# Kernel optimization log

Hardware: AMD Instinct MI355X
Metric: run time of the kernel (lower is better)

## Reference

```python
import jax, jax.numpy as jnp
import numpy as np

N, E = 50000, 800000
C, A_ALL, RAD_IN, FC1, FC2 = 128, 256, 32, 64, 64
H, AH, VH = 8, 16, 16  # heads, alpha channels/head, value channels/head


def _radial_mlp(x, w1, b1, w2, b2, w3, b3):
    x = jax.nn.silu(x @ w1 + b1)
    x = jax.nn.silu(x @ w2 + b2)
    return x @ w3 + b3


def _smooth_leaky_relu(x, a=0.2):
    # Equiformer SmoothLeakyReLU: 0.5*(1+a)*x + 0.5*(1-a)*x*(2*sigmoid(x)-1)
    return 0.5 * (1.0 + a) * x + 0.5 * (1.0 - a) * x * (2.0 * jax.nn.sigmoid(x) - 1.0)


def _segment_softmax(scores, seg, num_segments):
    m = jax.ops.segment_max(scores, seg, num_segments=num_segments)
    m = jnp.where(jnp.isfinite(m), m, 0.0)
    e = jnp.exp(scores - m[seg])
    s = jax.ops.segment_sum(e, seg, num_segments=num_segments)
    return e / (s[seg] + 1e-16)


def setup_inputs():
    key = jax.random.key(0)
    ks = jax.random.split(key, 16)

    def g(k, shape):
        scale = 1.0 / np.sqrt(shape[0])
        return jax.random.normal(k, shape, dtype=jnp.float32) * scale

    return {
        "node_input": jax.random.normal(ks[0], (N, C), dtype=jnp.float32),
        "node_attr": jnp.ones((N, 1), jnp.float32),
        "edge_attr": jax.random.uniform(ks[1], (E, 1), dtype=jnp.float32),
        "edge_scalars": jax.random.normal(ks[2], (E, RAD_IN), dtype=jnp.float32),
        "edge_src": jax.random.randint(ks[3], (E,), 0, N, dtype=jnp.int32),
        "edge_dst": jax.random.randint(ks[4], (E,), 0, N, dtype=jnp.int32),
        "batch": jnp.zeros((N,), jnp.int32),
        "w_src": g(ks[5], (C, C)), "b_src": jnp.zeros((C,), jnp.float32),
        "w_dst": g(ks[6], (C, C)),
        "fc_w1": g(ks[7], (RAD_IN, FC1)), "fc_b1": jnp.zeros((FC1,), jnp.float32),
        "fc_w2": g(ks[8], (FC1, FC2)), "fc_b2": jnp.zeros((FC2,), jnp.float32),
        "fc_w3": g(ks[9], (FC2, C)), "fc_b3": jnp.zeros((C,), jnp.float32),
        "w_sep": g(ks[10], (C, A_ALL)), "b_sep": jnp.zeros((A_ALL,), jnp.float32),
        "alpha_dot": jax.random.normal(ks[11], (1, H, AH), dtype=jnp.float32) * np.sqrt(2.0 / (H * AH)),
        "w_proj": g(ks[12], (H * VH, C)), "b_proj": jnp.zeros((C,), jnp.float32),
    }


def reference(node_input, node_attr, edge_attr, edge_scalars, edge_src, edge_dst, batch,
              w_src, b_src, w_dst, fc_w1, fc_b1, fc_w2, fc_b2, fc_w3, fc_b3,
              w_sep, b_sep, alpha_dot, w_proj, b_proj):
    n_nodes = node_input.shape[0]
    n_edges = edge_src.shape[0]
    # merge_src / merge_dst (LinearRS; bias only on src)
    msg_src = node_input @ w_src + b_src                     # [N, C]
    msg_dst = node_input @ w_dst                             # [N, C]
    message = msg_src[edge_src] + msg_dst[edge_dst]          # [E, C] edge gather
    # SeparableFCTP: radial-weighted depthwise tensor product (scalar irreps)
    rad_w = _radial_mlp(edge_scalars, fc_w1, fc_b1, fc_w2, fc_b2, fc_w3, fc_b3)  # [E, C]
    message = message * edge_attr * rad_w                    # depthwise TP
    message = message @ w_sep + b_sep                        # [E, A_ALL] linear to attn_all
    # Vec2AttnHeads + split alpha/value per head
    msg_h = message.reshape(n_edges, H, AH + VH)
    alpha = _smooth_leaky_relu(msg_h[:, :, :AH])             # [E, H, AH]
    value = msg_h[:, :, AH:]                                 # [E, H, VH]
    score = jnp.einsum('ehk,ahk->eh', alpha, alpha_dot)      # [E, H]
    att = _segment_softmax(score, edge_dst, n_nodes)[..., None]
    out = jax.ops.segment_sum(value * att, edge_dst, num_segments=n_nodes)  # scatter-add
    out = out.reshape(n_nodes, H * VH)                       # AttnHeads2Vec
    return out @ w_proj + b_proj
```

## Files before the change

kernel.cpp:

```cpp
#include <hip/hip_runtime.h>

#define NN 50000
#define NE 800000

typedef unsigned short u16;
typedef __bf16 bf16x8 __attribute__((ext_vector_type(8)));
typedef float f32x4 __attribute__((ext_vector_type(4)));

__device__ __forceinline__ u16 f2b(float f){
  unsigned x = __float_as_uint(f);
  return (u16)((x + 0x7FFFu + ((x>>16)&1u)) >> 16);
}
#define MFMA16(a,b,c) __builtin_amdgcn_mfma_f32_16x16x32_bf16((a),(b),(c),0,0,0)

__global__ void k_prep(const float* __restrict__ w1, const float* __restrict__ w2,
                       const float* __restrict__ w3, const float* __restrict__ wsep,
                       const float* __restrict__ wsrc, const float* __restrict__ wdst,
                       const float* __restrict__ wproj,
                       u16* __restrict__ w1T, u16* __restrict__ w2T,
                       u16* __restrict__ w3T, u16* __restrict__ wsepT,
                       u16* __restrict__ wsrcT, u16* __restrict__ wdstT,
                       u16* __restrict__ wprojT)
{
  int id = blockIdx.x*256 + threadIdx.x;
  if (id < 2048)  { int n=id>>5,  k=id&31;  w1T[id]   = f2b(w1[k*64+n]);    return; } id -= 2048;
  if (id < 4096)  { int n=id>>6,  k=id&63;  w2T[id]   = f2b(w2[k*64+n]);    return; } id -= 4096;
  if (id < 8192)  { int n=id>>6,  k=id&63;  w3T[id]   = f2b(w3[k*128+n]);   return; } id -= 8192;
  if (id < 32768) { int n=id>>7,  k=id&127; wsepT[id] = f2b(wsep[k*256+n]); return; } id -= 32768;
  if (id < 16384) { int n=id>>7,  k=id&127; wsrcT[id] = f2b(wsrc[k*128+n]); return; } id -= 16384;
  if (id < 16384) { int n=id>>7,  k=id&127; wdstT[id] = f2b(wdst[k*128+n]); return; } id -= 16384;
  if (id < 16384) { int n=id>>7,  k=id&127; wprojT[id]= f2b(wproj[k*128+n]); return; }
}

__launch_bounds__(256)
__global__ void k_node(const float* __restrict__ x, const u16* __restrict__ wsrcT,
                       const u16* __restrict__ wdstT, const float* __restrict__ bsrc,
                       float* __restrict__ msgsrc, float* __restrict__ msgdst)
{
  __shared__ u16 sX[64*136];
  __shared__ u16 sW[128*136];
  __shared__ float sB[128];
  const int tid = threadIdx.x;
  const int n0 = blockIdx.x*64;
  for (int idx = tid; idx < 64*32; idx += 256){
    int r = idx>>5, s = idx&31;
    float4 v = make_float4(0.f,0.f,0.f,0.f);
    if (n0 + r < NN) v = *(const float4*)(x + (size_t)(n0+r)*128 + s*4);
    ushort4 o; o.x=f2b(v.x); o.y=f2b(v.y); o.z=f2b(v.z); o.w=f2b(v.w);
    *(ushort4*)(&sX[r*136 + s*4]) = o;
  }
  const int wave = tid>>6, lane = tid&63, l15 = lane&15, q = lane>>4;
  for (int half = 0; half < 2; ++half){
    const u16* wT = half ? wdstT : wsrcT;
    for (int idx = tid; idx < 128*16; idx += 256){
      int r = idx>>4, s = idx&15;
      *(uint4*)(&sW[r*136 + s*8]) = *(const uint4*)(wT + r*128 + s*8);
    }
    if (tid < 128) sB[tid] = half ? 0.0f : bsrc[tid];
    __syncthreads();
    f32x4 acc[8];
    #pragma unroll
    for (int n=0;n<8;++n) acc[n] = (f32x4){0.f,0.f,0.f,0.f};
    #pragma unroll
    for (int k0=0;k0<128;k0+=32){
      bf16x8 a = *(const bf16x8*)(&sX[(wave*16+l15)*136 + k0 + q*8]);
      #pragma unroll
      for (int n=0;n<8;++n){
        bf16x8 b = *(const bf16x8*)(&sW[(n*16+l15)*136 + k0 + q*8]);
        acc[n] = MFMA16(a,b,acc[n]);
      }
    }
    float* outp = half ? msgdst : msgsrc;
    #pragma unroll
    for (int n=0;n<8;++n){
      #pragma unroll
      for (int r=0;r<4;++r){
        int row = n0 + wave*16 + q*4 + r;
        if (row < NN) outp[(size_t)row*128 + n*16 + l15] = acc[n][r] + sB[n*16+l15];
      }
    }
    __syncthreads();
  }
}

#define PM 136
#define PH 72
#define PX 40
__launch_bounds__(256)
__global__ void k_edge(const float* __restrict__ escal, const float* __restrict__ eattr,
                       const int* __restrict__ esrc, const int* __restrict__ edst,
                       const float* __restrict__ msgsrc, const float* __restrict__ msgdst,
                       const u16* __restrict__ w1T, const u16* __restrict__ w2T,
                       const u16* __restrict__ w3T, const u16* __restrict__ wsepT,
                       const float* __restrict__ b1, const float* __restrict__ b2,
                       const float* __restrict__ b3, const float* __restrict__ bsep,
                       const float* __restrict__ adot,
                       float* __restrict__ num, float* __restrict__ denom)
{
  __shared__ __attribute__((aligned(16))) char pool[49408];
  u16*   sXs  = (u16*)(pool + 0);
  u16*   sW1  = (u16*)(pool + 5120);
  u16*   sW2  = (u16*)(pool + 10240);
  u16*   sH1  = (u16*)(pool + 19456);
  u16*   sMsg = (u16*)(pool + 28672);
  float* sB1  = (float*)(pool + 46080);
  float* sB2  = (float*)(pool + 46336);
  float* sB3  = (float*)(pool + 46592);
  float* sBs  = (float*)(pool + 47104);
  float* sAD  = (float*)(pool + 48128);
  float* sEA  = (float*)(pool + 48640);
  int*   sSrc = (int*)(pool + 48896);
  int*   sDst = (int*)(pool + 49152);
  u16*   sH2  = (u16*)(pool + 0);
  u16*   sW3C = (u16*)(pool + 10240);
  u16*   sWsp = (u16*)(pool + 10240);

  const int tid = threadIdx.x;
  const int e0 = blockIdx.x*64;
  const int wave = tid>>6, lane = tid&63, l15 = lane&15, q = lane>>4;

  {
    for (int j = tid; j < 512; j += 256){ int r=j>>3, s=j&7;
      float4 v = *(const float4*)(escal + (size_t)(e0+r)*32 + s*4);
      ushort4 o; o.x=f2b(v.x); o.y=f2b(v.y); o.z=f2b(v.z); o.w=f2b(v.w);
      *(ushort4*)&sXs[r*PX + s*4] = o; }
    if (tid < 256){ int r=tid>>2, s=tid&3;
      *(uint4*)&sW1[r*PX + s*8] = *(const uint4*)(w1T + r*32 + s*8); }
    for (int j = tid; j < 512; j += 256){ int r=j>>3, s=j&7;
      *(uint4*)&sW2[r*PH + s*8] = *(const uint4*)(w2T + r*64 + s*8); }
    if (tid < 64)  sB1[tid] = b1[tid];
    if (tid < 64)  sB2[tid] = b2[tid];
    if (tid < 128) sB3[tid] = b3[tid];
    sBs[tid] = bsep[tid];
    if (tid < 128) sAD[tid] = adot[tid];
    if (tid < 64){ sEA[tid] = eattr[e0+tid]; sSrc[tid] = esrc[e0+tid]; sDst[tid] = edst[e0+tid]; }
  }
  __syncthreads();

  {
    f32x4 acc[4];
    #pragma unroll
    for (int n=0;n<4;++n) acc[n] = (f32x4){0.f,0.f,0.f,0.f};
    bf16x8 a = *(const bf16x8*)&sXs[(wave*16+l15)*PX + q*8];
    #pragma unroll
    for (int n=0;n<4;++n){
      bf16x8 b = *(const bf16x8*)&sW1[(n*16+l15)*PX + q*8];
      acc[n] = MFMA16(a,b,acc[n]);
    }
    #pragma unroll
    for (int n=0;n<4;++n){
      #pragma unroll
      for (int r=0;r<4;++r){
        float v = acc[n][r] + sB1[n*16+l15];
        float h = v / (1.0f + __expf(-v));
        sH1[(wave*16+q*4+r)*PH + n*16+l15] = f2b(h);
      }
    }
  }
  __syncthreads();

  {
    f32x4 acc[4];
    #pragma unroll
    for (int n=0;n<4;++n) acc[n] = (f32x4){0.f,0.f,0.f,0.f};
    #pragma unroll
    for (int k0=0;k0<64;k0+=32){
      bf16x8 a = *(const bf16x8*)&sH1[(wave*16+l15)*PH + k0 + q*8];
      #pragma unroll
      for (int n=0;n<4;++n){
        bf16x8 b = *(const bf16x8*)&sW2[(n*16+l15)*PH + k0 + q*8];
        acc[n] = MFMA16(a,b,acc[n]);
      }
    }
    #pragma unroll
    for (int n=0;n<4;++n){
      #pragma unroll
      for (int r=0;r<4;++r){
        float v = acc[n][r] + sB2[n*16+l15];
        float h = v / (1.0f + __expf(-v));
        sH2[(wave*16+q*4+r)*PH + n*16+l15] = f2b(h);
      }
    }
  }
  __syncthreads();

  for (int ch=0; ch<2; ++ch){
    for (int j = tid; j < 512; j += 256){ int r=j>>3, s=j&7;
      *(uint4*)&sW3C[r*PH + s*8] = *(const uint4*)(w3T + (size_t)(ch*64+r)*64 + s*8); }
    __syncthreads();
    const int m0 = (wave&1)*2, n0 = (wave>>1)*2;
    f32x4 acc[2][2];
    #pragma unroll
    for (int mm=0;mm<2;++mm)
      #pragma unroll
      for (int nn=0;nn<2;++nn) acc[mm][nn] = (f32x4){0.f,0.f,0.f,0.f};
    #pragma unroll
    for (int k0=0;k0<64;k0+=32){
      bf16x8 a0 = *(const bf16x8*)&sH2[((m0  )*16+l15)*PH + k0 + q*8];
      bf16x8 a1 = *(const bf16x8*)&sH2[((m0+1)*16+l15)*PH + k0 + q*8];
      bf16x8 b0 = *(const bf16x8*)&sW3C[((n0  )*16+l15)*PH + k0 + q*8];
      bf16x8 b1 = *(const bf16x8*)&sW3C[((n0+1)*16+l15)*PH + k0 + q*8];
      acc[0][0] = MFMA16(a0,b0,acc[0][0]);
      acc[1][0] = MFMA16(a1,b0,acc[1][0]);
      acc[0][1] = MFMA16(a0,b1,acc[0][1]);
      acc[1][1] = MFMA16(a1,b1,acc[1][1]);
    }
    #pragma unroll
    for (int mm=0;mm<2;++mm){
      #pragma unroll
      for (int nn=0;nn<2;++nn){
        int c = ch*64 + (n0+nn)*16 + l15;
        #pragma unroll
        for (int r=0;r<4;++r){
          float v = acc[mm][nn][r] + sB3[c];
          sMsg[((m0+mm)*16+q*4+r)*PM + c] = f2b(v);
        }
      }
    }
    __syncthreads();
  }

  for (int idx = tid; idx < 64*32; idx += 256){
    int r = idx>>5, s = idx&31;
    int cs = s*4;
    float4 a4 = *(const float4*)(msgsrc + (size_t)sSrc[r]*128 + cs);
    float4 d4 = *(const float4*)(msgdst + (size_t)sDst[r]*128 + cs);
    float ea = sEA[r];
    ushort4 rw = *(ushort4*)&sMsg[r*PM + cs];
    ushort4 o;
    o.x = f2b((a4.x + d4.x) * ea * __uint_as_float(((unsigned)rw.x)<<16));
    o.y = f2b((a4.y + d4.y) * ea * __uint_as_float(((unsigned)rw.y)<<16));
    o.z = f2b((a4.z + d4.z) * ea * __uint_as_float(((unsigned)rw.z)<<16));
    o.w = f2b((a4.w + d4.w) * ea * __uint_as_float(((unsigned)rw.w)<<16));
    *(ushort4*)&sMsg[r*PM + cs] = o;
  }
  __syncthreads();

  const int fm0 = (wave&1)*2, fn0 = (wave>>1)*2;
  for (int ch=0; ch<4; ++ch){
    for (int j = tid; j < 1024; j += 256){ int r=j>>4, s=j&15;
      *(uint4*)&sWsp[r*PM + s*8] = *(const uint4*)(wsepT + (size_t)(ch*64+r)*128 + s*8); }
    __syncthreads();
    f32x4 acc[2][2];
    #pragma unroll
    for (int mm=0;mm<2;++mm)
      #pragma unroll
      for (int nn=0;nn<2;++nn) acc[mm][nn] = (f32x4){0.f,0.f,0.f,0.f};
    #pragma unroll
    for (int k0=0;k0<128;k0+=32){
      bf16x8 a0 = *(const bf16x8*)&sMsg[((fm0  )*16+l15)*PM + k0 + q*8];
      bf16x8 a1 = *(const bf16x8*)&sMsg[((fm0+1)*16+l15)*PM + k0 + q*8];
      bf16x8 b0 = *(const bf16x8*)&sWsp[((fn0  )*16+l15)*PM + k0 + q*8];
      bf16x8 b1 = *(const bf16x8*)&sWsp[((fn0+1)*16+l15)*PM + k0 + q*8];
      acc[0][0] = MFMA16(a0,b0,acc[0][0]);
      acc[1][0] = MFMA16(a1,b0,acc[1][0]);
      acc[0][1] = MFMA16(a0,b1,acc[0][1]);
      acc[1][1] = MFMA16(a1,b1,acc[1][1]);
    }
    {
      const int h  = ch*2 + (fn0>>1);
      const int ca = ch*64 + fn0*16;
      const float ba = sBs[ca + l15];
      const float bv = sBs[ca + 16 + l15];
      const float ad = sAD[h*16 + l15];
      #pragma unroll
      for (int mm=0;mm<2;++mm){
        #pragma unroll
        for (int r=0;r<4;++r){
          int eloc = (fm0+mm)*16 + q*4 + r;
          float av  = acc[mm][0][r] + ba;
          float sig = 1.0f/(1.0f + __expf(-av));
          float sl  = av*(0.2f + 0.8f*sig);
          float contrib = sl * ad;
          contrib += __shfl_xor(contrib, 1);
          contrib += __shfl_xor(contrib, 2);
          contrib += __shfl_xor(contrib, 4);
          contrib += __shfl_xor(contrib, 8);
          float w  = __expf(contrib);
          int dst  = sDst[eloc];
          float vv = acc[mm][1][r] + bv;
          unsafeAtomicAdd(&num[(size_t)dst*128 + h*16 + l15], w*vv);
          if (l15 == 0) unsafeAtomicAdd(&denom[(size_t)dst*8 + h], w);
        }
      }
    }
    __syncthreads();
  }
}

__launch_bounds__(256)
__global__ void k_out(const float* __restrict__ num, const float* __restrict__ denom,
                      const u16* __restrict__ wprojT, const float* __restrict__ bproj,
                      float* __restrict__ out)
{
  __shared__ u16 sX[64*136];
  __shared__ u16 sW[128*136];
  __shared__ float sB[128];
  const int tid = threadIdx.x;
  const int n0 = blockIdx.x*64;
  for (int idx = tid; idx < 64*128; idx += 256){
    int r = idx>>7, c = idx&127;
    float xv = 0.f;
    int row = n0 + r;
    if (row < NN){
      float d = denom[row*8 + (c>>4)];
      xv = num[(size_t)row*128 + c] / (d + 1e-16f);
    }
    sX[r*136 + c] = f2b(xv);
  }
  for (int idx = tid; idx < 128*16; idx += 256){ int r=idx>>4, s=idx&15;
    *(uint4*)&sW[r*136 + s*8] = *(const uint4*)(wprojT + r*128 + s*8); }
  if (tid < 128) sB[tid] = bproj[tid];
  __syncthreads();
  const int wave = tid>>6, lane = tid&63, l15 = lane&15, q = lane>>4;
  f32x4 acc[8];
  #pragma unroll
  for (int n=0;n<8;++n) acc[n] = (f32x4){0.f,0.f,0.f,0.f};
  #pragma unroll
  for (int k0=0;k0<128;k0+=32){
    bf16x8 a = *(const bf16x8*)&sX[(wave*16+l15)*136 + k0 + q*8];
    #pragma unroll
    for (int n=0;n<8;++n){
      bf16x8 b = *(const bf16x8*)&sW[(n*16+l15)*136 + k0 + q*8];
      acc[n] = MFMA16(a,b,acc[n]);
    }
  }
  #pragma unroll
  for (int n=0;n<8;++n){
    #pragma unroll
    for (int r=0;r<4;++r){
      int row = n0 + wave*16 + q*4 + r;
      if (row < NN) out[(size_t)row*128 + n*16 + l15] = acc[n][r] + sB[n*16+l15];
    }
  }
}

extern "C" void kernel_launch(void* const* d_in, const int* in_sizes, int n_in,
                              void* d_out, int out_size, void* d_ws, size_t ws_size,
                              hipStream_t stream)
{
  const float* node_input = (const float*)d_in[0];
  const float* eattr = (const float*)d_in[2];
  const float* escal = (const float*)d_in[3];
  const int*   esrc  = (const int*)d_in[4];
  const int*   edst  = (const int*)d_in[5];
  const float* wsrc  = (const float*)d_in[7];
  const float* bsrc  = (const float*)d_in[8];
  const float* wdst  = (const float*)d_in[9];
  const float* w1    = (const float*)d_in[10];
  const float* b1    = (const float*)d_in[11];
  const float* w2    = (const float*)d_in[12];
  const float* b2    = (const float*)d_in[13];
  const float* w3    = (const float*)d_in[14];
  const float* b3    = (const float*)d_in[15];
  const float* wsep  = (const float*)d_in[16];
  const float* bsep  = (const float*)d_in[17];
  const float* adot  = (const float*)d_in[18];
  const float* wproj = (const float*)d_in[19];
  const float* bproj = (const float*)d_in[20];

  char* ws = (char*)d_ws;
  size_t off = 0;
  auto alloc = [&](size_t bytes)->void*{ void* p = ws + off; off += (bytes + 255) & ~(size_t)255; return p; };
  float* msgsrc = (float*)alloc((size_t)NN*128*4);
  float* msgdst = (float*)alloc((size_t)NN*128*4);
  float* num    = (float*)alloc((size_t)NN*128*4);
  float* denom  = (float*)alloc((size_t)NN*8*4);
  u16* w1T    = (u16*)alloc(2048*2);
  u16* w2T    = (u16*)alloc(4096*2);
  u16* w3T    = (u16*)alloc(8192*2);
  u16* wsepT  = (u16*)alloc(32768*2);
  u16* wsrcT  = (u16*)alloc(16384*2);
  u16* wdstT  = (u16*)alloc(16384*2);
  u16* wprojT = (u16*)alloc(16384*2);

  hipMemsetAsync(num,   0, (size_t)NN*128*4, stream);
  hipMemsetAsync(denom, 0, (size_t)NN*8*4,   stream);

  k_prep<<<376, 256, 0, stream>>>(w1,w2,w3,wsep,wsrc,wdst,wproj,
                                  w1T,w2T,w3T,wsepT,wsrcT,wdstT,wprojT);
  k_node<<<782, 256, 0, stream>>>(node_input, wsrcT, wdstT, bsrc, msgsrc, msgdst);
  k_edge<<<12500, 256, 0, stream>>>(escal, eattr, esrc, edst, msgsrc, msgdst,
                                    w1T, w2T, w3T, wsepT, b1, b2, b3, bsep, adot,
                                    num, denom);
  k_out<<<782, 256, 0, stream>>>(num, denom, wprojT, bproj, (float*)d_out);
}
```

Before: 912.8 us.

## Read edge-kernel weights from global memory and shrink LDS for occupancy

Weight matrices, biases and edge index/attr arrays are no longer staged in shared memory. MFMA B operands and biases now come straight from global/L2, which cuts LDS from about 48KB to 26KB and removes several per-chunk __syncthreads. Launch bounds now request 6 blocks per SM to raise occupancy. In exchange, weights are loaded redundantly from global by every wave, and the register cap may cause spills.

```diff
diff --git a/kernel.cpp b/kernel.cpp
--- a/kernel.cpp
+++ b/kernel.cpp
@@ -86,7 +86,7 @@
 #define PM 136
 #define PH 72
 #define PX 40
-__launch_bounds__(256)
+__launch_bounds__(256,6)
 __global__ void k_edge(const float* __restrict__ escal, const float* __restrict__ eattr,
                        const int* __restrict__ esrc, const int* __restrict__ edst,
                        const float* __restrict__ msgsrc, const float* __restrict__ msgdst,
@@ -97,44 +97,20 @@
                        const float* __restrict__ adot,
                        float* __restrict__ num, float* __restrict__ denom)
 {
-  __shared__ __attribute__((aligned(16))) char pool[49408];
-  u16*   sXs  = (u16*)(pool + 0);
-  u16*   sW1  = (u16*)(pool + 5120);
-  u16*   sW2  = (u16*)(pool + 10240);
-  u16*   sH1  = (u16*)(pool + 19456);
-  u16*   sMsg = (u16*)(pool + 28672);
-  float* sB1  = (float*)(pool + 46080);
-  float* sB2  = (float*)(pool + 46336);
-  float* sB3  = (float*)(pool + 46592);
-  float* sBs  = (float*)(pool + 47104);
-  float* sAD  = (float*)(pool + 48128);
-  float* sEA  = (float*)(pool + 48640);
-  int*   sSrc = (int*)(pool + 48896);
-  int*   sDst = (int*)(pool + 49152);
-  u16*   sH2  = (u16*)(pool + 0);
-  u16*   sW3C = (u16*)(pool + 10240);
-  u16*   sWsp = (u16*)(pool + 10240);
+  __shared__ __attribute__((aligned(16))) char pool[26624];
+  u16* sH1  = (u16*)(pool + 0);
+  u16* sXs  = (u16*)(pool + 9216);
+  u16* sH2  = (u16*)(pool + 17408);
+  u16* sMsg = (u16*)(pool + 0);
 
   const int tid = threadIdx.x;
   const int e0 = blockIdx.x*64;
   const int wave = tid>>6, lane = tid&63, l15 = lane&15, q = lane>>4;
 
-  {
-    for (int j = tid; j < 512; j += 256){ int r=j>>3, s=j&7;
-      float4 v = *(const float4*)(escal + (size_t)(e0+r)*32 + s*4);
-      ushort4 o; o.x=f2b(v.x); o.y=f2b(v.y); o.z=f2b(v.z); o.w=f2b(v.w);
-      *(ushort4*)&sXs[r*PX + s*4] = o; }
-    if (tid < 256){ int r=tid>>2, s=tid&3;
-      *(uint4*)&sW1[r*PX + s*8] = *(const uint4*)(w1T + r*32 + s*8); }
-    for (int j = tid; j < 512; j += 256){ int r=j>>3, s=j&7;
-      *(uint4*)&sW2[r*PH + s*8] = *(const uint4*)(w2T + r*64 + s*8); }
-    if (tid < 64)  sB1[tid] = b1[tid];
-    if (tid < 64)  sB2[tid] = b2[tid];
-    if (tid < 128) sB3[tid] = b3[tid];
-    sBs[tid] = bsep[tid];
-    if (tid < 128) sAD[tid] = adot[tid];
-    if (tid < 64){ sEA[tid] = eattr[e0+tid]; sSrc[tid] = esrc[e0+tid]; sDst[tid] = edst[e0+tid]; }
-  }
+  for (int j = tid; j < 512; j += 256){ int r=j>>3, s=j&7;
+    float4 v = *(const float4*)(escal + (size_t)(e0+r)*32 + s*4);
+    ushort4 o; o.x=f2b(v.x); o.y=f2b(v.y); o.z=f2b(v.z); o.w=f2b(v.w);
+    *(ushort4*)&sXs[r*PX + s*4] = o; }
   __syncthreads();
 
   {
@@ -144,14 +120,15 @@
     bf16x8 a = *(const bf16x8*)&sXs[(wave*16+l15)*PX + q*8];
     #pragma unroll
     for (int n=0;n<4;++n){
-      bf16x8 b = *(const bf16x8*)&sW1[(n*16+l15)*PX + q*8];
+      bf16x8 b = *(const bf16x8*)(w1T + (n*16+l15)*32 + q*8);
       acc[n] = MFMA16(a,b,acc[n]);
     }
     #pragma unroll
     for (int n=0;n<4;++n){
+      float bia = b1[n*16+l15];
       #pragma unroll
       for (int r=0;r<4;++r){
-        float v = acc[n][r] + sB1[n*16+l15];
+        float v = acc[n][r] + bia;
         float h = v / (1.0f + __expf(-v));
         sH1[(wave*16+q*4+r)*PH + n*16+l15] = f2b(h);
       }
@@ -168,15 +145,16 @@
       bf16x8 a = *(const bf16x8*)&sH1[(wave*16+l15)*PH + k0 + q*8];
       #pragma unroll
       for (int n=0;n<4;++n){
-        bf16x8 b = *(const bf16x8*)&sW2[(n*16+l15)*PH + k0 + q*8];
+        bf16x8 b = *(const bf16x8*)(w2T + (n*16+l15)*64 + k0 + q*8);
         acc[n] = MFMA16(a,b,acc[n]);
       }
     }
     #pragma unroll
     for (int n=0;n<4;++n){
+      float bia = b2[n*16+l15];
       #pragma unroll
       for (int r=0;r<4;++r){
-        float v = acc[n][r] + sB2[n*16+l15];
+        float v = acc[n][r] + bia;
         float h = v / (1.0f + __expf(-v));
         sH2[(wave*16+q*4+r)*PH + n*16+l15] = f2b(h);
       }
@@ -184,48 +162,51 @@
   }
   __syncthreads();
 
-  for (int ch=0; ch<2; ++ch){
-    for (int j = tid; j < 512; j += 256){ int r=j>>3, s=j&7;
-      *(uint4*)&sW3C[r*PH + s*8] = *(const uint4*)(w3T + (size_t)(ch*64+r)*64 + s*8); }
-    __syncthreads();
+  {
     const int m0 = (wave&1)*2, n0 = (wave>>1)*2;
-    f32x4 acc[2][2];
-    #pragma unroll
-    for (int mm=0;mm<2;++mm)
-      #pragma unroll
-      for (int nn=0;nn<2;++nn) acc[mm][nn] = (f32x4){0.f,0.f,0.f,0.f};
-    #pragma unroll
-    for (int k0=0;k0<64;k0+=32){
-      bf16x8 a0 = *(const bf16x8*)&sH2[((m0  )*16+l15)*PH + k0 + q*8];
-      bf16x8 a1 = *(const bf16x8*)&sH2[((m0+1)*16+l15)*PH + k0 + q*8];
-      bf16x8 b0 = *(const bf16x8*)&sW3C[((n0  )*16+l15)*PH + k0 + q*8];
-      bf16x8 b1 = *(const bf16x8*)&sW3C[((n0+1)*16+l15)*PH + k0 + q*8];
-      acc[0][0] = MFMA16(a0,b0,acc[0][0]);
-      acc[1][0] = MFMA16(a1,b0,acc[1][0]);
-      acc[0][1] = MFMA16(a0,b1,acc[0][1]);
-      acc[1][1] = MFMA16(a1,b1,acc[1][1]);
-    }
-    #pragma unroll
-    for (int mm=0;mm<2;++mm){
-      #pragma unroll
-      for (int nn=0;nn<2;++nn){
-        int c = ch*64 + (n0+nn)*16 + l15;
+    #pragma unroll
+    for (int ch=0; ch<2; ++ch){
+      f32x4 acc[2][2];
+      #pragma unroll
+      for (int mm=0;mm<2;++mm)
         #pragma unroll
-        for (int r=0;r<4;++r){
-          float v = acc[mm][nn][r] + sB3[c];
-          sMsg[((m0+mm)*16+q*4+r)*PM + c] = f2b(v);
+        for (int nn=0;nn<2;++nn) acc[mm][nn] = (f32x4){0.f,0.f,0.f,0.f};
+      const u16* w3b = w3T + (size_t)(ch*64)*64;
+      #pragma unroll
+      for (int k0=0;k0<64;k0+=32){
+        bf16x8 a0 = *(const bf16x8*)&sH2[((m0  )*16+l15)*PH + k0 + q*8];
+        bf16x8 a1 = *(const bf16x8*)&sH2[((m0+1)*16+l15)*PH + k0 + q*8];
+        bf16x8 bb0 = *(const bf16x8*)(w3b + ((n0  )*16+l15)*64 + k0 + q*8);
+        bf16x8 bb1 = *(const bf16x8*)(w3b + ((n0+1)*16+l15)*64 + k0 + q*8);
+        acc[0][0] = MFMA16(a0,bb0,acc[0][0]);
+        acc[1][0] = MFMA16(a1,bb0,acc[1][0]);
+        acc[0][1] = MFMA16(a0,bb1,acc[0][1]);
+        acc[1][1] = MFMA16(a1,bb1,acc[1][1]);
+      }
+      #pragma unroll
+      for (int mm=0;mm<2;++mm){
+        #pragma unroll
+        for (int nn=0;nn<2;++nn){
+          int c = ch*64 + (n0+nn)*16 + l15;
+          float bia = b3[c];
+          #pragma unroll
+          for (int r=0;r<4;++r){
+            float v = acc[mm][nn][r] + bia;
+            sMsg[((m0+mm)*16+q*4+r)*PM + c] = f2b(v);
+          }
         }
       }
     }
-    __syncthreads();
-  }
+  }
+  __syncthreads();
 
   for (int idx = tid; idx < 64*32; idx += 256){
     int r = idx>>5, s = idx&31;
     int cs = s*4;
-    float4 a4 = *(const float4*)(msgsrc + (size_t)sSrc[r]*128 + cs);
-    float4 d4 = *(const float4*)(msgdst + (size_t)sDst[r]*128 + cs);
-    float ea = sEA[r];
+    int is = esrc[e0+r], id = edst[e0+r];
+    float4 a4 = *(const float4*)(msgsrc + (size_t)is*128 + cs);
+    float4 d4 = *(const float4*)(msgdst + (size_t)id*128 + cs);
+    float ea = eattr[e0+r];
     ushort4 rw = *(ushort4*)&sMsg[r*PM + cs];
     ushort4 o;
     o.x = f2b((a4.x + d4.x) * ea * __uint_as_float(((unsigned)rw.x)<<16));
@@ -236,55 +217,56 @@
   }
   __syncthreads();
 
-  const int fm0 = (wave&1)*2, fn0 = (wave>>1)*2;
-  for (int ch=0; ch<4; ++ch){
-    for (int j = tid; j < 1024; j += 256){ int r=j>>4, s=j&15;
-      *(uint4*)&sWsp[r*PM + s*8] = *(const uint4*)(wsepT + (size_t)(ch*64+r)*128 + s*8); }
-    __syncthreads();
-    f32x4 acc[2][2];
-    #pragma unroll
-    for (int mm=0;mm<2;++mm)
-      #pragma unroll
-      for (int nn=0;nn<2;++nn) acc[mm][nn] = (f32x4){0.f,0.f,0.f,0.f};
-    #pragma unroll
-    for (int k0=0;k0<128;k0+=32){
-      bf16x8 a0 = *(const bf16x8*)&sMsg[((fm0  )*16+l15)*PM + k0 + q*8];
-      bf16x8 a1 = *(const bf16x8*)&sMsg[((fm0+1)*16+l15)*PM + k0 + q*8];
-      bf16x8 b0 = *(const bf16x8*)&sWsp[((fn0  )*16+l15)*PM + k0 + q*8];
-      bf16x8 b1 = *(const bf16x8*)&sWsp[((fn0+1)*16+l15)*PM + k0 + q*8];
-      acc[0][0] = MFMA16(a0,b0,acc[0][0]);
-      acc[1][0] = MFMA16(a1,b0,acc[1][0]);
-      acc[0][1] = MFMA16(a0,b1,acc[0][1]);
-      acc[1][1] = MFMA16(a1,b1,acc[1][1]);
-    }
-    {
-      const int h  = ch*2 + (fn0>>1);
-      const int ca = ch*64 + fn0*16;
-      const float ba = sBs[ca + l15];
-      const float bv = sBs[ca + 16 + l15];
-      const float ad = sAD[h*16 + l15];
-      #pragma unroll
-      for (int mm=0;mm<2;++mm){
+  {
+    const int fm0 = (wave&1)*2, fn0 = (wave>>1)*2;
+    const u16* wb0 = wsepT + (size_t)((fn0  )*16+l15)*128 + q*8;
+    const u16* wb1 = wsepT + (size_t)((fn0+1)*16+l15)*128 + q*8;
+    #pragma unroll
+    for (int ch=0; ch<4; ++ch){
+      f32x4 acc[2][2];
+      #pragma unroll
+      for (int mm=0;mm<2;++mm)
         #pragma unroll
-        for (int r=0;r<4;++r){
-          int eloc = (fm0+mm)*16 + q*4 + r;
-          float av  = acc[mm][0][r] + ba;
-          float sig = 1.0f/(1.0f + __expf(-av));
-          float sl  = av*(0.2f + 0.8f*sig);
-          float contrib = sl * ad;
-          contrib += __shfl_xor(contrib, 1);
-          contrib += __shfl_xor(contrib, 2);
-          contrib += __shfl_xor(contrib, 4);
-          contrib += __shfl_xor(contrib, 8);
-          float w  = __expf(contrib);
-          int dst  = sDst[eloc];
-          float vv = acc[mm][1][r] + bv;
-          unsafeAtomicAdd(&num[(size_t)dst*128 + h*16 + l15], w*vv);
-          if (l15 == 0) unsafeAtomicAdd(&denom[(size_t)dst*8 + h], w);
+        for (int nn=0;nn<2;++nn) acc[mm][nn] = (f32x4){0.f,0.f,0.f,0.f};
+      #pragma unroll
+      for (int k0=0;k0<128;k0+=32){
+        bf16x8 a0 = *(const bf16x8*)&sMsg[((fm0  )*16+l15)*PM + k0 + q*8];
+        bf16x8 a1 = *(const bf16x8*)&sMsg[((fm0+1)*16+l15)*PM + k0 + q*8];
+        bf16x8 bb0 = *(const bf16x8*)(wb0 + (size_t)ch*64*128 + k0);
+        bf16x8 bb1 = *(const bf16x8*)(wb1 + (size_t)ch*64*128 + k0);
+        acc[0][0] = MFMA16(a0,bb0,acc[0][0]);
+        acc[1][0] = MFMA16(a1,bb0,acc[1][0]);
+        acc[0][1] = MFMA16(a0,bb1,acc[0][1]);
+        acc[1][1] = MFMA16(a1,bb1,acc[1][1]);
+      }
+      {
+        const int h  = ch*2 + (fn0>>1);
+        const int ca = ch*64 + fn0*16;
+        const float ba = bsep[ca + l15];
+        const float bv = bsep[ca + 16 + l15];
+        const float ad = adot[h*16 + l15];
+        #pragma unroll
+        for (int mm=0;mm<2;++mm){
+          #pragma unroll
+          for (int r=0;r<4;++r){
+            int eloc = (fm0+mm)*16 + q*4 + r;
+            float av  = acc[mm][0][r] + ba;
+            float sig = 1.0f/(1.0f + __expf(-av));
+            float sl  = av*(0.2f + 0.8f*sig);
+            float contrib = sl * ad;
+            contrib += __shfl_xor(contrib, 1);
+            contrib += __shfl_xor(contrib, 2);
+            contrib += __shfl_xor(contrib, 4);
+            contrib += __shfl_xor(contrib, 8);
+            float w  = __expf(contrib);
+            int dst  = edst[e0 + eloc];
+            float vv = acc[mm][1][r] + bv;
+            unsafeAtomicAdd(&num[(size_t)dst*128 + h*16 + l15], w*vv);
+            if (l15 == 0) unsafeAtomicAdd(&denom[(size_t)dst*8 + h], w);
+          }
         }
       }
     }
-    __syncthreads();
   }
 }
 
```

After: 1.022 ms. 12.0% more time.
